# Performance work log

Hardware: AMD Instinct MI355X
Metric: run time of the kernel (lower is better)

The kernel has to match this reference:

```python
import jax, jax.numpy as jnp
import numpy as np

B, N, H, D, MAXH, MRP = 64, 197, 12, 64, 16, 14  # batch, tokens (14x14+cls), heads, head_dim, supernet max heads, max rel pos
TABLE = 2 * MRP + 2  # 30 rows per table


def setup_inputs() -> dict:
    key = jax.random.key(0)
    ks = jax.random.split(key, 5)
    x = jax.random.normal(ks[0], (B, N, 3 * D * MAXH), dtype=jnp.float32)
    mk = lambda k: (0.02 * jax.random.normal(k, (TABLE, D), dtype=jnp.float32))
    return {"x": x, "tk_v": mk(ks[1]), "tk_h": mk(ks[2]), "tv_v": mk(ks[3]), "tv_h": mk(ks[4])}


def _rel_pos_emb(table_v, table_h, n):
    # RelativePosition2D_super.forward(length_q=n, length_k=n)
    lq = n - 1
    s = int(np.sqrt(lq))  # 14
    r = jnp.arange(lq)
    dv = r[None, :] // s - r[:, None] // s
    dh = r[None, :] % s - r[:, None] % s
    iv = jnp.clip(dv, -MRP, MRP) + MRP + 1
    ih = jnp.clip(dh, -MRP, MRP) + MRP + 1
    iv = jnp.pad(iv, ((1, 0), (1, 0)))  # CLS row/col -> index 0
    ih = jnp.pad(ih, ((1, 0), (1, 0)))
    return table_v[iv] + table_h[ih]  # (n, n, D)


def reference(x, tk_v, tk_h, tv_v, tv_h):
    scale = D ** (-0.5)  # sample_scale = 64**-0.5
    xs = x[:, :, : H * D * 3]
    qkv = xs.reshape(B, N, 3, H, D).transpose(2, 0, 3, 1, 4)  # (3,B,H,N,D)
    q, k, v = qkv[0], qkv[1], qkv[2]
    attn = jnp.einsum('bhid,bhjd->bhij', q, k) * scale
    rk = _rel_pos_emb(tk_v, tk_h, N)  # (N,N,D)
    attn = attn + jnp.einsum('bhid,ijd->bhij', q, rk) * scale
    attn = jax.nn.softmax(attn, axis=-1)  # attn_drop p=0.0 -> identity
    out = jnp.einsum('bhij,bhjd->bhid', attn, v)
    rv = _rel_pos_emb(tv_v, tv_h, N)  # (N,N,D)
    out = out + jnp.einsum('bhij,ijd->bhid', attn, rv)
    out = out.transpose(0, 2, 1, 3).reshape(B, N, H * D)  # (B,N,768)
    return jnp.pad(out, ((0, 0), (0, 0), (0, MAXH * D - H * D)))  # pad to (B,N,1024)
```

## Files before the change

kernel.cpp:

```cpp
#include <hip/hip_runtime.h>

typedef float  f4v   __attribute__((ext_vector_type(4)));
typedef float  f32x4 __attribute__((ext_vector_type(4)));
typedef short  s8v   __attribute__((ext_vector_type(8)));
typedef short  s4v   __attribute__((ext_vector_type(4)));
typedef __bf16 bf16x8 __attribute__((ext_vector_type(8)));

#define N_   197
#define H_   12
#define CIN  3072
#define COUT 1024
#define VSTR 296
#define ASTR 72
#define BSTR 40

#define MEMBAR() asm volatile("" ::: "memory")

__device__ __forceinline__ unsigned short f2bf(float f) {
    unsigned u = __float_as_uint(f);
    u += 0x7FFFu + ((u >> 16) & 1u);
    return (unsigned short)(u >> 16);
}
__device__ __forceinline__ float bf2f(unsigned short s) {
    return __uint_as_float(((unsigned)s) << 16);
}
__device__ __forceinline__ f32x4 mfma_bf16(s8v a, s8v b, f32x4 c) {
    return __builtin_amdgcn_mfma_f32_16x16x32_bf16(
        __builtin_bit_cast(bf16x8, a), __builtin_bit_cast(bf16x8, b), c, 0, 0, 0);
}
__device__ __forceinline__ void st4f(volatile unsigned short* p, float a, float b, float c, float d) {
    s4v v;
    v[0] = (short)f2bf(a); v[1] = (short)f2bf(b);
    v[2] = (short)f2bf(c); v[3] = (short)f2bf(d);
    *(volatile s4v*)p = v;
}
__device__ __forceinline__ void st4z(volatile unsigned short* p) {
    s4v v = {0, 0, 0, 0};
    *(volatile s4v*)p = v;
}

__launch_bounds__(1024, 4)
__global__ void attn_super(const float* __restrict__ x,
                           const float* __restrict__ tkv,
                           const float* __restrict__ tkh,
                           const float* __restrict__ tvv,
                           const float* __restrict__ tvh,
                           float* __restrict__ out) {
    __shared__ __align__(16) unsigned short Kl[272 * 72];
    __shared__ __align__(16) unsigned short Vt[64 * VSTR];
    __shared__ __align__(16) unsigned short AR[16][16 * ASTR];
    __shared__ __align__(16) unsigned short INDv[16 * 224];
    __shared__ __align__(16) unsigned short INDh[16 * 224];
    __shared__ __align__(16) unsigned short Bext[224 * BSTR];

    const int bid = blockIdx.x;
    const int b = bid / H_, h = bid % H_;
    const int tid = threadIdx.x;
    const int w  = tid >> 6;
    const int l  = tid & 63;
    const int lg = l >> 4;
    const int ln = l & 15;

    const float* xb = x + (size_t)b * N_ * CIN;

    if (h < 4) {
        float* oz = out + (size_t)b * N_ * COUT + 768 + h * 64;
        for (int idx = tid; idx < N_ * 16; idx += 1024) {
            int row = idx >> 4, c4 = idx & 15;
            f4v z = {0.f, 0.f, 0.f, 0.f};
            *(f4v*)(oz + (size_t)row * COUT + c4 * 4) = z;
        }
    }

    f4v kr[5];
    #pragma unroll
    for (int it = 0; it < 5; ++it) {
        int idx = it * 1024 + tid;
        bool a5 = (it < 4) || (tid < 256);
        int row = idx >> 4, d0 = (idx & 15) * 4;
        f4v v = {0.f, 0.f, 0.f, 0.f};
        if (a5) {
            if (row < N_)                     v = *(const f4v*)(xb + (size_t)row * CIN + 768 + h * 64 + d0);
            else if (row >= 208 && row < 238) v = *(const f4v*)(tkv + (row - 208) * 64 + d0);
            else if (row >= 240 && row < 270) v = *(const f4v*)(tkh + (row - 240) * 64 + d0);
        }
        kr[it] = v;
    }
    f4v q1[2], q2[2];
    if (w < 13) {
        int qrow = w * 16 + ln; if (qrow > 196) qrow = 196;
        const float* qp = xb + (size_t)qrow * CIN + h * 64;
        #pragma unroll
        for (int s2 = 0; s2 < 2; ++s2) {
            q1[s2] = *(const f4v*)(qp + s2 * 32 + lg * 8);
            q2[s2] = *(const f4v*)(qp + s2 * 32 + lg * 8 + 4);
        }
    }
    f4v vr[5];
    #pragma unroll
    for (int it = 0; it < 5; ++it) {
        int idx = it * 1024 + tid;
        bool a5 = (it < 4) || (tid < 512);
        int j = idx % 288, d0 = (idx / 288) * 4;
        f4v v = {0.f, 0.f, 0.f, 0.f};
        if (a5) {
            if (j < N_)                     v = *(const f4v*)(xb + (size_t)j * CIN + 1536 + h * 64 + d0);
            else if (j >= 224 && j < 254)   v = *(const f4v*)(tvv + (j - 224) * 64 + d0);
            else if (j >= 256 && j < 286)   v = *(const f4v*)(tvh + (j - 256) * 64 + d0);
        }
        vr[it] = v;
    }

    #pragma unroll
    for (int it = 0; it < 5; ++it) {
        int idx = it * 1024 + tid;
        bool a5 = (it < 4) || (tid < 256);
        if (a5) {
            int row = idx >> 4, d0 = (idx & 15) * 4;
            f4v v = kr[it];
            s4v pk;
            pk[0] = (short)f2bf(v[0]); pk[1] = (short)f2bf(v[1]);
            pk[2] = (short)f2bf(v[2]); pk[3] = (short)f2bf(v[3]);
            *(s4v*)(&Kl[row * 72 + d0]) = pk;
        }
    }
    for (int idx = tid; idx < 16 * 224; idx += 1024) {
        int m = idx / 224, k = idx % 224;
        int km1 = k - 1;
        bool kv = (k >= 1 && k <= 196);
        INDv[idx] = (kv && (km1 / 14) == m) ? (unsigned short)0x3F80 : (unsigned short)0;
        INDh[idx] = (kv && (km1 % 14) == m) ? (unsigned short)0x3F80 : (unsigned short)0;
    }
    for (int idx = tid; idx < 224 * 32; idx += 1024) {
        int k = idx >> 5, c = idx & 31;
        unsigned short v = 0;
        if (k >= 1 && k <= 196) {
            int mj = (k - 1) / 14, cj = (k - 1) - mj * 14;
            if (c == mj || c == 16 + cj) v = (unsigned short)0x3F80;
        } else if (k == 0) {
            if (c == 15 || c == 31) v = (unsigned short)0x3F80;
        }
        Bext[k * BSTR + c] = v;
    }
    __syncthreads();

    const int tile = w, qb = tile * 16;
    const unsigned short* ar = &AR[w][0];
    volatile unsigned short* arv = &AR[w][0];

    f32x4 S[13];
    float rsq[4], p0q[4];
    int ritq[4], citq[4];
    if (w < 13) {
        const int iL  = qb + ln;
        const int im1 = (iL > 0) ? iL - 1 : 0;
        const int rit = im1 / 14;
        const int cit = im1 - rit * 14;

        s8v aq[2];
        #pragma unroll
        for (int s2 = 0; s2 < 2; ++s2) {
            #pragma unroll
            for (int e = 0; e < 4; ++e) {
                aq[s2][e]     = (short)f2bf(q1[s2][e] * 0.125f);
                aq[s2][e + 4] = (short)f2bf(q2[s2][e] * 0.125f);
            }
        }
        float spv = 0.f, sph = 0.f;
        #pragma unroll
        for (int tt = 0; tt < 4; ++tt) {
            f32x4 acc = {0.f, 0.f, 0.f, 0.f};
            #pragma unroll
            for (int s2 = 0; s2 < 2; ++s2) {
                const s8v bk = *(const s8v*)(&Kl[((13 + tt) * 16 + ln) * 72 + s2 * 32 + lg * 8]);
                acc = mfma_bf16(bk, aq[s2], acc);
            }
            const bool isV  = (tt < 2);
            const int mbase = (tt & 1) * 16;
            const int shift = isV ? rit : cit;
            const int cbase = isV ? 0 : 16;
            const bool skip0 = (tile == 0 && ln == 0);
            #pragma unroll
            for (int r = 0; r < 4; ++r) {
                int m = mbase + 4 * lg + r;
                int t = m + shift - 15;
                if (!skip0 && m < 30 && t >= 0 && t < 15)
                    arv[ln * ASTR + cbase + t] = f2bf(acc[r]);
                if (!skip0 && m == 0)
                    arv[ln * ASTR + cbase + 15] = f2bf(acc[r]);
            }
            if (tile == 0 && l == 0) {
                if (tt == 0) spv = acc[0];
                if (tt == 2) sph = acc[0];
            }
        }
        if (tile == 0 && l == 0) {
            unsigned short v0 = f2bf(spv), h0 = f2bf(sph);
            #pragma unroll
            for (int t = 0; t < 16; ++t) {
                arv[t] = v0;
                arv[16 + t] = h0;
            }
        }
        MEMBAR();
        const s8v aq2 = *(const s8v*)(&ar[ln * ASTR + lg * 8]);
        #pragma unroll
        for (int ct = 0; ct < 13; ++ct) {
            const s8v be = *(const s8v*)(&Bext[(ct * 16 + ln) * BSTR + lg * 8]);
            f32x4 acc = {0.f, 0.f, 0.f, 0.f};
            acc = mfma_bf16(be, aq2, acc);
            #pragma unroll
            for (int s2 = 0; s2 < 2; ++s2) {
                const s8v bk = *(const s8v*)(&Kl[(ct * 16 + ln) * 72 + s2 * 32 + lg * 8]);
                acc = mfma_bf16(bk, aq[s2], acc);
            }
            S[ct] = acc;
        }
    }
    #pragma unroll
    for (int it = 0; it < 5; ++it) {
        int idx = it * 1024 + tid;
        bool a5 = (it < 4) || (tid < 512);
        if (a5) {
            int j = idx % 288, d0 = (idx / 288) * 4;
            f4v v = vr[it];
            #pragma unroll
            for (int e = 0; e < 4; ++e)
                Vt[(d0 + e) * VSTR + j] = f2bf(v[e]);
        }
    }

    if (w < 13) {
        float rs4[4] = {0.f, 0.f, 0.f, 0.f};
        #pragma unroll
        for (int ct = 0; ct < 13; ++ct) {
            #pragma unroll
            for (int r = 0; r < 4; ++r) {
                float p = __expf(S[ct][r]);
                if (ct == 12) { if (4 * lg + r > 4) p = 0.f; }
                S[ct][r] = p;
                rs4[r] += p;
            }
        }
        float rs = (rs4[0] + rs4[1]) + (rs4[2] + rs4[3]);
        rs += __shfl_xor(rs, 16);
        rs += __shfl_xor(rs, 32);
        float p00 = S[0][0];
        #pragma unroll
        for (int r = 0; r < 4; ++r) {
            rsq[r] = __shfl(rs,  4 * lg + r);
            p0q[r] = __shfl(p00, 4 * lg + r);
        }
        #pragma unroll
        for (int r = 0; r < 4; ++r) {
            int qr2 = qb + 4 * lg + r;
            int im  = (qr2 > 0) ? qr2 - 1 : 0;
            ritq[r] = im / 14;
            citq[r] = im - ritq[r] * 14;
        }
    }
    __syncthreads();

    if (w >= 13) return;

    f32x4 oacc[4];
    #pragma unroll
    for (int nt = 0; nt < 4; ++nt) { f32x4 z = {0.f,0.f,0.f,0.f}; oacc[nt] = z; }
    f32x4 cwv = {0.f,0.f,0.f,0.f}, cwh = {0.f,0.f,0.f,0.f};

    #pragma unroll
    for (int win = 0; win < 3; ++win) {
        MEMBAR();
        #pragma unroll
        for (int cc = 0; cc < 4; ++cc) {
            int ct = win * 4 + cc;
            st4f(&arv[ln * ASTR + cc * 16 + 4 * lg], S[ct][0], S[ct][1], S[ct][2], S[ct][3]);
        }
        MEMBAR();
        #pragma unroll
        for (int kk = 0; kk < 2; ++kk) {
            int kt = win * 2 + kk;
            const s8v ap = *(const s8v*)(&ar[ln * ASTR + kk * 32 + lg * 8]);
            #pragma unroll
            for (int nt = 0; nt < 4; ++nt) {
                const s8v bv = *(const s8v*)(&Vt[(nt * 16 + ln) * VSTR + kt * 32 + lg * 8]);
                oacc[nt] = mfma_bf16(ap, bv, oacc[nt]);
            }
            const s8v bi = *(const s8v*)(&INDv[ln * 224 + kt * 32 + lg * 8]);
            cwv = mfma_bf16(ap, bi, cwv);
            const s8v bh = *(const s8v*)(&INDh[ln * 224 + kt * 32 + lg * 8]);
            cwh = mfma_bf16(ap, bh, cwh);
        }
    }
    {
        MEMBAR();
        st4f(&arv[ln * ASTR + 4 * lg], S[12][0], S[12][1], S[12][2], S[12][3]);
        st4z(&arv[ln * ASTR + 16 + 4 * lg]);
        st4z(&arv[ln * ASTR + 32 + lg * 8]);
        st4z(&arv[ln * ASTR + 36 + lg * 8]);
        MEMBAR();
        {
            const s8v ap = *(const s8v*)(&ar[ln * ASTR + lg * 8]);
            #pragma unroll
            for (int nt = 0; nt < 4; ++nt) {
                const s8v bv = *(const s8v*)(&Vt[(nt * 16 + ln) * VSTR + 192 + lg * 8]);
                oacc[nt] = mfma_bf16(ap, bv, oacc[nt]);
            }
            const s8v bi = *(const s8v*)(&INDv[ln * 224 + 192 + lg * 8]);
            cwv = mfma_bf16(ap, bi, cwv);
            const s8v bh = *(const s8v*)(&INDh[ln * 224 + 192 + lg * 8]);
            cwh = mfma_bf16(ap, bh, cwh);
        }
        MEMBAR();
        #pragma unroll
        for (int r = 0; r < 4; ++r) {
            int q = 4 * lg + r;
            bool isRow0 = (tile == 0) && (q == 0);
            if (ln <= 13 && !isRow0)
                arv[q * ASTR + 47 + ln - ritq[r]] = f2bf(cwv[r]);
            if (ln == 15)
                arv[q * ASTR + 32] = f2bf(isRow0 ? rsq[r] : p0q[r]);
        }
        MEMBAR();
        {
            const s8v ap = *(const s8v*)(&ar[ln * ASTR + 32 + lg * 8]);
            #pragma unroll
            for (int nt = 0; nt < 4; ++nt) {
                const s8v bv = *(const s8v*)(&Vt[(nt * 16 + ln) * VSTR + 224 + lg * 8]);
                oacc[nt] = mfma_bf16(ap, bv, oacc[nt]);
            }
        }
    }
    {
        MEMBAR();
        st4z(&arv[ln * ASTR + lg * 8]);
        st4z(&arv[ln * ASTR + 4 + lg * 8]);
        MEMBAR();
        #pragma unroll
        for (int r = 0; r < 4; ++r) {
            int q = 4 * lg + r;
            bool isRow0 = (tile == 0) && (q == 0);
            if (ln <= 13 && !isRow0)
                arv[q * ASTR + 15 + ln - citq[r]] = f2bf(cwh[r]);
            if (ln == 15)
                arv[q * ASTR + 0] = f2bf(isRow0 ? rsq[r] : p0q[r]);
        }
        MEMBAR();
        {
            const s8v ap = *(const s8v*)(&ar[ln * ASTR + lg * 8]);
            #pragma unroll
            for (int nt = 0; nt < 4; ++nt) {
                const s8v bv = *(const s8v*)(&Vt[(nt * 16 + ln) * VSTR + 256 + lg * 8]);
                oacc[nt] = mfma_bf16(ap, bv, oacc[nt]);
            }
        }
    }
    #pragma unroll
    for (int r = 0; r < 4; ++r) {
        int n = qb + 4 * lg + r;
        if (n < N_) {
            float sc = 1.0f / rsq[r];
            float* orow = out + ((size_t)b * N_ + n) * COUT + h * 64;
            #pragma unroll
            for (int nt = 0; nt < 4; ++nt)
                orow[nt * 16 + ln] = oacc[nt][r] * sc;
        }
    }
}

extern "C" void kernel_launch(void* const* d_in, const int* in_sizes, int n_in,
                              void* d_out, int out_size, void* d_ws, size_t ws_size,
                              hipStream_t stream) {
    const float* x   = (const float*)d_in[0];
    const float* tkv = (const float*)d_in[1];
    const float* tkh = (const float*)d_in[2];
    const float* tvv = (const float*)d_in[3];
    const float* tvh = (const float*)d_in[4];
    float* o = (float*)d_out;
    attn_super<<<dim3(64 * H_), dim3(1024), 0, stream>>>(x, tkv, tkh, tvv, tvh, o);
}
```

Measured before the change: 71.65 us.

## Make attention kernel persistent with prefetch of next head's Q/K/V

```diff
diff --git a/kernel.cpp b/kernel.cpp
--- a/kernel.cpp
+++ b/kernel.cpp
@@ -24,14 +24,17 @@
 __device__ __forceinline__ float bf2f(unsigned short s) {
     return __uint_as_float(((unsigned)s) << 16);
 }
+__device__ __forceinline__ unsigned pk2(float a, float b) {
+    return (unsigned)f2bf(a) | ((unsigned)f2bf(b) << 16);
+}
 __device__ __forceinline__ f32x4 mfma_bf16(s8v a, s8v b, f32x4 c) {
     return __builtin_amdgcn_mfma_f32_16x16x32_bf16(
         __builtin_bit_cast(bf16x8, a), __builtin_bit_cast(bf16x8, b), c, 0, 0, 0);
 }
-__device__ __forceinline__ void st4f(volatile unsigned short* p, float a, float b, float c, float d) {
+__device__ __forceinline__ void st4p(volatile unsigned short* p, unsigned u0, unsigned u1) {
     s4v v;
-    v[0] = (short)f2bf(a); v[1] = (short)f2bf(b);
-    v[2] = (short)f2bf(c); v[3] = (short)f2bf(d);
+    v[0] = (short)(u0 & 0xFFFF); v[1] = (short)(u0 >> 16);
+    v[2] = (short)(u1 & 0xFFFF); v[3] = (short)(u1 >> 16);
     *(volatile s4v*)p = v;
 }
 __device__ __forceinline__ void st4z(volatile unsigned short* p) {
@@ -54,76 +57,12 @@
     __shared__ __align__(16) unsigned short Bext[224 * BSTR];
 
     const int bid = blockIdx.x;
-    const int b = bid / H_, h = bid % H_;
     const int tid = threadIdx.x;
     const int w  = tid >> 6;
     const int l  = tid & 63;
     const int lg = l >> 4;
     const int ln = l & 15;
 
-    const float* xb = x + (size_t)b * N_ * CIN;
-
-    if (h < 4) {
-        float* oz = out + (size_t)b * N_ * COUT + 768 + h * 64;
-        for (int idx = tid; idx < N_ * 16; idx += 1024) {
-            int row = idx >> 4, c4 = idx & 15;
-            f4v z = {0.f, 0.f, 0.f, 0.f};
-            *(f4v*)(oz + (size_t)row * COUT + c4 * 4) = z;
-        }
-    }
-
-    f4v kr[5];
-    #pragma unroll
-    for (int it = 0; it < 5; ++it) {
-        int idx = it * 1024 + tid;
-        bool a5 = (it < 4) || (tid < 256);
-        int row = idx >> 4, d0 = (idx & 15) * 4;
-        f4v v = {0.f, 0.f, 0.f, 0.f};
-        if (a5) {
-            if (row < N_)                     v = *(const f4v*)(xb + (size_t)row * CIN + 768 + h * 64 + d0);
-            else if (row >= 208 && row < 238) v = *(const f4v*)(tkv + (row - 208) * 64 + d0);
-            else if (row >= 240 && row < 270) v = *(const f4v*)(tkh + (row - 240) * 64 + d0);
-        }
-        kr[it] = v;
-    }
-    f4v q1[2], q2[2];
-    if (w < 13) {
-        int qrow = w * 16 + ln; if (qrow > 196) qrow = 196;
-        const float* qp = xb + (size_t)qrow * CIN + h * 64;
-        #pragma unroll
-        for (int s2 = 0; s2 < 2; ++s2) {
-            q1[s2] = *(const f4v*)(qp + s2 * 32 + lg * 8);
-            q2[s2] = *(const f4v*)(qp + s2 * 32 + lg * 8 + 4);
-        }
-    }
-    f4v vr[5];
-    #pragma unroll
-    for (int it = 0; it < 5; ++it) {
-        int idx = it * 1024 + tid;
-        bool a5 = (it < 4) || (tid < 512);
-        int j = idx % 288, d0 = (idx / 288) * 4;
-        f4v v = {0.f, 0.f, 0.f, 0.f};
-        if (a5) {
-            if (j < N_)                     v = *(const f4v*)(xb + (size_t)j * CIN + 1536 + h * 64 + d0);
-            else if (j >= 224 && j < 254)   v = *(const f4v*)(tvv + (j - 224) * 64 + d0);
-            else if (j >= 256 && j < 286)   v = *(const f4v*)(tvh + (j - 256) * 64 + d0);
-        }
-        vr[it] = v;
-    }
-
-    #pragma unroll
-    for (int it = 0; it < 5; ++it) {
-        int idx = it * 1024 + tid;
-        bool a5 = (it < 4) || (tid < 256);
-        if (a5) {
-            int row = idx >> 4, d0 = (idx & 15) * 4;
-            f4v v = kr[it];
-            s4v pk;
-            pk[0] = (short)f2bf(v[0]); pk[1] = (short)f2bf(v[1]);
-            pk[2] = (short)f2bf(v[2]); pk[3] = (short)f2bf(v[3]);
-            *(s4v*)(&Kl[row * 72 + d0]) = pk;
-        }
-    }
     for (int idx = tid; idx < 16 * 224; idx += 1024) {
         int m = idx / 224, k = idx % 224;
         int km1 = k - 1;
@@ -142,229 +81,366 @@
         }
         Bext[k * BSTR + c] = v;
     }
+
+    f4v kr[5];
+    f4v q1[2], q2[2];
+    f4v vr[5];
+    {
+        int pair = bid;
+        int b = pair / H_, h = pair - b * H_;
+        const float* xb = x + (size_t)b * N_ * CIN;
+        #pragma unroll
+        for (int it = 0; it < 5; ++it) {
+            int idx = it * 1024 + tid;
+            bool a5 = (it < 4) || (tid < 256);
+            int row = idx >> 4, d0 = (idx & 15) * 4;
+            f4v v = {0.f, 0.f, 0.f, 0.f};
+            if (a5) {
+                if (row < N_)                     v = *(const f4v*)(xb + (size_t)row * CIN + 768 + h * 64 + d0);
+                else if (row >= 208 && row < 238) v = *(const f4v*)(tkv + (row - 208) * 64 + d0);
+                else if (row >= 240 && row < 270) v = *(const f4v*)(tkh + (row - 240) * 64 + d0);
+            }
+            kr[it] = v;
+        }
+        if (w < 13) {
+            int qrow = w * 16 + ln; if (qrow > 196) qrow = 196;
+            const float* qp = xb + (size_t)qrow * CIN + h * 64;
+            #pragma unroll
+            for (int s2 = 0; s2 < 2; ++s2) {
+                q1[s2] = *(const f4v*)(qp + s2 * 32 + lg * 8);
+                q2[s2] = *(const f4v*)(qp + s2 * 32 + lg * 8 + 4);
+            }
+        }
+        #pragma unroll
+        for (int it = 0; it < 5; ++it) {
+            int idx = it * 1024 + tid;
+            bool a5 = (it < 4) || (tid < 256);
+            if (a5) {
+                int row = idx >> 4, d0 = (idx & 15) * 4;
+                f4v v = kr[it];
+                s4v pk;
+                pk[0] = (short)f2bf(v[0]); pk[1] = (short)f2bf(v[1]);
+                pk[2] = (short)f2bf(v[2]); pk[3] = (short)f2bf(v[3]);
+                *(s4v*)(&Kl[row * 72 + d0]) = pk;
+            }
+        }
+        #pragma unroll
+        for (int it = 0; it < 5; ++it) {
+            int idx = it * 1024 + tid;
+            bool a5 = (it < 4) || (tid < 512);
+            int j = idx % 288, d0 = (idx / 288) * 4;
+            f4v v = {0.f, 0.f, 0.f, 0.f};
+            if (a5) {
+                if (j < N_)                     v = *(const f4v*)(xb + (size_t)j * CIN + 1536 + h * 64 + d0);
+                else if (j >= 224 && j < 254)   v = *(const f4v*)(tvv + (j - 224) * 64 + d0);
+                else if (j >= 256 && j < 286)   v = *(const f4v*)(tvh + (j - 256) * 64 + d0);
+            }
+            vr[it] = v;
+        }
+    }
     __syncthreads();
 
     const int tile = w, qb = tile * 16;
     const unsigned short* ar = &AR[w][0];
     volatile unsigned short* arv = &AR[w][0];
 
-    f32x4 S[13];
-    float rsq[4], p0q[4];
-    int ritq[4], citq[4];
-    if (w < 13) {
-        const int iL  = qb + ln;
-        const int im1 = (iL > 0) ? iL - 1 : 0;
-        const int rit = im1 / 14;
-        const int cit = im1 - rit * 14;
-
-        s8v aq[2];
+    for (int i = 0; i < 3; ++i) {
+        const int pair = i * 256 + bid;
+        const int b = pair / H_, h = pair - b * H_;
+        const float* xb = x + (size_t)b * N_ * CIN;
+
+        if (h < 4) {
+            float* oz = out + (size_t)b * N_ * COUT + 768 + h * 64;
+            for (int idx = tid; idx < N_ * 16; idx += 1024) {
+                int row = idx >> 4, c4 = idx & 15;
+                f4v z = {0.f, 0.f, 0.f, 0.f};
+                *(f4v*)(oz + (size_t)row * COUT + c4 * 4) = z;
+            }
+        }
+
+        unsigned pp[13][2];
+        float rsq[4], p0q[4];
+        int ritq[4], citq[4];
+
+        if (w < 13) {
+            const int iL  = qb + ln;
+            const int im1 = (iL > 0) ? iL - 1 : 0;
+            const int rit = im1 / 14;
+            const int cit = im1 - rit * 14;
+
+            s8v aq[2];
+            #pragma unroll
+            for (int s2 = 0; s2 < 2; ++s2) {
+                #pragma unroll
+                for (int e = 0; e < 4; ++e) {
+                    aq[s2][e]     = (short)f2bf(q1[s2][e] * 0.125f);
+                    aq[s2][e + 4] = (short)f2bf(q2[s2][e] * 0.125f);
+                }
+            }
+            float spv = 0.f, sph = 0.f;
+            #pragma unroll
+            for (int tt = 0; tt < 4; ++tt) {
+                f32x4 acc = {0.f, 0.f, 0.f, 0.f};
+                #pragma unroll
+                for (int s2 = 0; s2 < 2; ++s2) {
+                    const s8v bk = *(const s8v*)(&Kl[((13 + tt) * 16 + ln) * 72 + s2 * 32 + lg * 8]);
+                    acc = mfma_bf16(bk, aq[s2], acc);
+                }
+                const bool isV  = (tt < 2);
+                const int mbase = (tt & 1) * 16;
+                const int shift = isV ? rit : cit;
+                const int cbase = isV ? 0 : 16;
+                const bool skip0 = (tile == 0 && ln == 0);
+                #pragma unroll
+                for (int r = 0; r < 4; ++r) {
+                    int m = mbase + 4 * lg + r;
+                    int t = m + shift - 15;
+                    if (!skip0 && m < 30 && t >= 0 && t < 15)
+                        arv[ln * ASTR + cbase + t] = f2bf(acc[r]);
+                    if (!skip0 && m == 0)
+                        arv[ln * ASTR + cbase + 15] = f2bf(acc[r]);
+                }
+                if (tile == 0 && l == 0) {
+                    if (tt == 0) spv = acc[0];
+                    if (tt == 2) sph = acc[0];
+                }
+            }
+            if (tile == 0 && l == 0) {
+                unsigned short v0 = f2bf(spv), h0 = f2bf(sph);
+                #pragma unroll
+                for (int t = 0; t < 16; ++t) {
+                    arv[t] = v0;
+                    arv[16 + t] = h0;
+                }
+            }
+            MEMBAR();
+            const s8v aq2 = *(const s8v*)(&ar[ln * ASTR + lg * 8]);
+            f32x4 S[13];
+            #pragma unroll
+            for (int ct = 0; ct < 13; ++ct) {
+                const s8v be = *(const s8v*)(&Bext[(ct * 16 + ln) * BSTR + lg * 8]);
+                f32x4 acc = {0.f, 0.f, 0.f, 0.f};
+                acc = mfma_bf16(be, aq2, acc);
+                #pragma unroll
+                for (int s2 = 0; s2 < 2; ++s2) {
+                    const s8v bk = *(const s8v*)(&Kl[(ct * 16 + ln) * 72 + s2 * 32 + lg * 8]);
+                    acc = mfma_bf16(bk, aq[s2], acc);
+                }
+                S[ct] = acc;
+            }
+            float rs4[4] = {0.f, 0.f, 0.f, 0.f};
+            float p00 = 0.f;
+            #pragma unroll
+            for (int ct = 0; ct < 13; ++ct) {
+                float pv[4];
+                #pragma unroll
+                for (int r = 0; r < 4; ++r) {
+                    float p = __expf(S[ct][r]);
+                    if (ct == 12) { if (4 * lg + r > 4) p = 0.f; }
+                    pv[r] = p;
+                    rs4[r] += p;
+                }
+                if (ct == 0) p00 = pv[0];
+                pp[ct][0] = pk2(pv[0], pv[1]);
+                pp[ct][1] = pk2(pv[2], pv[3]);
+            }
+            float rs = (rs4[0] + rs4[1]) + (rs4[2] + rs4[3]);
+            rs += __shfl_xor(rs, 16);
+            rs += __shfl_xor(rs, 32);
+            #pragma unroll
+            for (int r = 0; r < 4; ++r) {
+                rsq[r] = __shfl(rs,  4 * lg + r);
+                p0q[r] = __shfl(p00, 4 * lg + r);
+            }
+            #pragma unroll
+            for (int r = 0; r < 4; ++r) {
+                int qr2 = qb + 4 * lg + r;
+                int im  = (qr2 > 0) ? qr2 - 1 : 0;
+                ritq[r] = im / 14;
+                citq[r] = im - ritq[r] * 14;
+            }
+        }
         #pragma unroll
-        for (int s2 = 0; s2 < 2; ++s2) {
-            #pragma unroll
-            for (int e = 0; e < 4; ++e) {
-                aq[s2][e]     = (short)f2bf(q1[s2][e] * 0.125f);
-                aq[s2][e + 4] = (short)f2bf(q2[s2][e] * 0.125f);
-            }
-        }
-        float spv = 0.f, sph = 0.f;
+        for (int it = 0; it < 5; ++it) {
+            int idx = it * 1024 + tid;
+            bool a5 = (it < 4) || (tid < 512);
+            if (a5) {
+                int j = idx % 288, d0 = (idx / 288) * 4;
+                f4v v = vr[it];
+                #pragma unroll
+                for (int e = 0; e < 4; ++e)
+                    Vt[(d0 + e) * VSTR + j] = f2bf(v[e]);
+            }
+        }
+        if (i < 2) {
+            const int np = (i + 1) * 256 + bid;
+            const int nb = np / H_, nh = np - nb * H_;
+            const float* nxb = x + (size_t)nb * N_ * CIN;
+            #pragma unroll
+            for (int it = 0; it < 5; ++it) {
+                int idx = it * 1024 + tid;
+                bool a5 = (it < 4) || (tid < 256);
+                int row = idx >> 4, d0 = (idx & 15) * 4;
+                f4v v = {0.f, 0.f, 0.f, 0.f};
+                if (a5) {
+                    if (row < N_)                     v = *(const f4v*)(nxb + (size_t)row * CIN + 768 + nh * 64 + d0);
+                    else if (row >= 208 && row < 238) v = *(const f4v*)(tkv + (row - 208) * 64 + d0);
+                    else if (row >= 240 && row < 270) v = *(const f4v*)(tkh + (row - 240) * 64 + d0);
+                }
+                kr[it] = v;
+            }
+            if (w < 13) {
+                int qrow = w * 16 + ln; if (qrow > 196) qrow = 196;
+                const float* qp = nxb + (size_t)qrow * CIN + nh * 64;
+                #pragma unroll
+                for (int s2 = 0; s2 < 2; ++s2) {
+                    q1[s2] = *(const f4v*)(qp + s2 * 32 + lg * 8);
+                    q2[s2] = *(const f4v*)(qp + s2 * 32 + lg * 8 + 4);
+                }
+            }
+        }
+        __syncthreads();
+
+        if (w < 13) {
+            f32x4 oacc[4];
+            #pragma unroll
+            for (int nt = 0; nt < 4; ++nt) { f32x4 z = {0.f,0.f,0.f,0.f}; oacc[nt] = z; }
+            f32x4 cwv = {0.f,0.f,0.f,0.f}, cwh = {0.f,0.f,0.f,0.f};
+
+            #pragma unroll
+            for (int win = 0; win < 3; ++win) {
+                MEMBAR();
+                #pragma unroll
+                for (int cc = 0; cc < 4; ++cc) {
+                    int ct = win * 4 + cc;
+                    st4p(&arv[ln * ASTR + cc * 16 + 4 * lg], pp[ct][0], pp[ct][1]);
+                }
+                MEMBAR();
+                #pragma unroll
+                for (int kk = 0; kk < 2; ++kk) {
+                    int kt = win * 2 + kk;
+                    const s8v ap = *(const s8v*)(&ar[ln * ASTR + kk * 32 + lg * 8]);
+                    #pragma unroll
+                    for (int nt = 0; nt < 4; ++nt) {
+                        const s8v bv = *(const s8v*)(&Vt[(nt * 16 + ln) * VSTR + kt * 32 + lg * 8]);
+                        oacc[nt] = mfma_bf16(ap, bv, oacc[nt]);
+                    }
+                    const s8v bi = *(const s8v*)(&INDv[ln * 224 + kt * 32 + lg * 8]);
+                    cwv = mfma_bf16(ap, bi, cwv);
+                    const s8v bh = *(const s8v*)(&INDh[ln * 224 + kt * 32 + lg * 8]);
+                    cwh = mfma_bf16(ap, bh, cwh);
+                }
+            }
+            {
+                MEMBAR();
+                st4p(&arv[ln * ASTR + 4 * lg], pp[12][0], pp[12][1]);
+                st4z(&arv[ln * ASTR + 16 + 4 * lg]);
+                st4z(&arv[ln * ASTR + 32 + lg * 8]);
+                st4z(&arv[ln * ASTR + 36 + lg * 8]);
+                MEMBAR();
+                {
+                    const s8v ap = *(const s8v*)(&ar[ln * ASTR + lg * 8]);
+                    #pragma unroll
+                    for (int nt = 0; nt < 4; ++nt) {
+                        const s8v bv = *(const s8v*)(&Vt[(nt * 16 + ln) * VSTR + 192 + lg * 8]);
+                        oacc[nt] = mfma_bf16(ap, bv, oacc[nt]);
+                    }
+                    const s8v bi = *(const s8v*)(&INDv[ln * 224 + 192 + lg * 8]);
+                    cwv = mfma_bf16(ap, bi, cwv);
+                    const s8v bh = *(const s8v*)(&INDh[ln * 224 + 192 + lg * 8]);
+                    cwh = mfma_bf16(ap, bh, cwh);
+                }
+                MEMBAR();
+                #pragma unroll
+                for (int r = 0; r < 4; ++r) {
+                    int q = 4 * lg + r;
+                    bool isRow0 = (tile == 0) && (q == 0);
+                    if (ln <= 13 && !isRow0)
+                        arv[q * ASTR + 47 + ln - ritq[r]] = f2bf(cwv[r]);
+                    if (ln == 15)
+                        arv[q * ASTR + 32] = f2bf(isRow0 ? rsq[r] : p0q[r]);
+                }
+                MEMBAR();
+                {
+                    const s8v ap = *(const s8v*)(&ar[ln * ASTR + 32 + lg * 8]);
+                    #pragma unroll
+                    for (int nt = 0; nt < 4; ++nt) {
+                        const s8v bv = *(const s8v*)(&Vt[(nt * 16 + ln) * VSTR + 224 + lg * 8]);
+                        oacc[nt] = mfma_bf16(ap, bv, oacc[nt]);
+                    }
+                }
+            }
+            {
+                MEMBAR();
+                st4z(&arv[ln * ASTR + lg * 8]);
+                st4z(&arv[ln * ASTR + 4 + lg * 8]);
+                MEMBAR();
+                #pragma unroll
+                for (int r = 0; r < 4; ++r) {
+                    int q = 4 * lg + r;
+                    bool isRow0 = (tile == 0) && (q == 0);
+                    if (ln <= 13 && !isRow0)
+                        arv[q * ASTR + 15 + ln - citq[r]] = f2bf(cwh[r]);
+                    if (ln == 15)
+                        arv[q * ASTR + 0] = f2bf(isRow0 ? rsq[r] : p0q[r]);
+                }
+                MEMBAR();
+                {
+                    const s8v ap = *(const s8v*)(&ar[ln * ASTR + lg * 8]);
+                    #pragma unroll
+                    for (int nt = 0; nt < 4; ++nt) {
+                        const s8v bv = *(const s8v*)(&Vt[(nt * 16 + ln) * VSTR + 256 + lg * 8]);
+                        oacc[nt] = mfma_bf16(ap, bv, oacc[nt]);
+                    }
+                }
+            }
+            #pragma unroll
+            for (int r = 0; r < 4; ++r) {
+                int n = qb + 4 * lg + r;
+                if (n < N_) {
+                    float sc = 1.0f / rsq[r];
+                    float* orow = out + ((size_t)b * N_ + n) * COUT + h * 64;
+                    #pragma unroll
+                    for (int nt = 0; nt < 4; ++nt)
+                        orow[nt * 16 + ln] = oacc[nt][r] * sc;
+                }
+            }
+        }
+
+        if (i == 2) break;
+
         #pragma unroll
-        for (int tt = 0; tt < 4; ++tt) {
-            f32x4 acc = {0.f, 0.f, 0.f, 0.f};
-            #pragma unroll
-            for (int s2 = 0; s2 < 2; ++s2) {
-                const s8v bk = *(const s8v*)(&Kl[((13 + tt) * 16 + ln) * 72 + s2 * 32 + lg * 8]);
-                acc = mfma_bf16(bk, aq[s2], acc);
-            }
-            const bool isV  = (tt < 2);
-            const int mbase = (tt & 1) * 16;
-            const int shift = isV ? rit : cit;
-            const int cbase = isV ? 0 : 16;
-            const bool skip0 = (tile == 0 && ln == 0);
-            #pragma unroll
-            for (int r = 0; r < 4; ++r) {
-                int m = mbase + 4 * lg + r;
-                int t = m + shift - 15;
-                if (!skip0 && m < 30 && t >= 0 && t < 15)
-                    arv[ln * ASTR + cbase + t] = f2bf(acc[r]);
-                if (!skip0 && m == 0)
-                    arv[ln * ASTR + cbase + 15] = f2bf(acc[r]);
-            }
-            if (tile == 0 && l == 0) {
-                if (tt == 0) spv = acc[0];
-                if (tt == 2) sph = acc[0];
-            }
-        }
-        if (tile == 0 && l == 0) {
-            unsigned short v0 = f2bf(spv), h0 = f2bf(sph);
-            #pragma unroll
-            for (int t = 0; t < 16; ++t) {
-                arv[t] = v0;
-                arv[16 + t] = h0;
-            }
-        }
-        MEMBAR();
-        const s8v aq2 = *(const s8v*)(&ar[ln * ASTR + lg * 8]);
-        #pragma unroll
-        for (int ct = 0; ct < 13; ++ct) {
-            const s8v be = *(const s8v*)(&Bext[(ct * 16 + ln) * BSTR + lg * 8]);
-            f32x4 acc = {0.f, 0.f, 0.f, 0.f};
-            acc = mfma_bf16(be, aq2, acc);
-            #pragma unroll
-            for (int s2 = 0; s2 < 2; ++s2) {
-                const s8v bk = *(const s8v*)(&Kl[(ct * 16 + ln) * 72 + s2 * 32 + lg * 8]);
-                acc = mfma_bf16(bk, aq[s2], acc);
-            }
-            S[ct] = acc;
-        }
-    }
-    #pragma unroll
-    for (int it = 0; it < 5; ++it) {
-        int idx = it * 1024 + tid;
-        bool a5 = (it < 4) || (tid < 512);
-        if (a5) {
-            int j = idx % 288, d0 = (idx / 288) * 4;
-            f4v v = vr[it];
-            #pragma unroll
-            for (int e = 0; e < 4; ++e)
-                Vt[(d0 + e) * VSTR + j] = f2bf(v[e]);
-        }
-    }
-
-    if (w < 13) {
-        float rs4[4] = {0.f, 0.f, 0.f, 0.f};
-        #pragma unroll
-        for (int ct = 0; ct < 13; ++ct) {
-            #pragma unroll
-            for (int r = 0; r < 4; ++r) {
-                float p = __expf(S[ct][r]);
-                if (ct == 12) { if (4 * lg + r > 4) p = 0.f; }
-                S[ct][r] = p;
-                rs4[r] += p;
-            }
-        }
-        float rs = (rs4[0] + rs4[1]) + (rs4[2] + rs4[3]);
-        rs += __shfl_xor(rs, 16);
-        rs += __shfl_xor(rs, 32);
-        float p00 = S[0][0];
-        #pragma unroll
-        for (int r = 0; r < 4; ++r) {
-            rsq[r] = __shfl(rs,  4 * lg + r);
-            p0q[r] = __shfl(p00, 4 * lg + r);
-        }
-        #pragma unroll
-        for (int r = 0; r < 4; ++r) {
-            int qr2 = qb + 4 * lg + r;
-            int im  = (qr2 > 0) ? qr2 - 1 : 0;
-            ritq[r] = im / 14;
-            citq[r] = im - ritq[r] * 14;
-        }
-    }
-    __syncthreads();
-
-    if (w >= 13) return;
-
-    f32x4 oacc[4];
-    #pragma unroll
-    for (int nt = 0; nt < 4; ++nt) { f32x4 z = {0.f,0.f,0.f,0.f}; oacc[nt] = z; }
-    f32x4 cwv = {0.f,0.f,0.f,0.f}, cwh = {0.f,0.f,0.f,0.f};
-
-    #pragma unroll
-    for (int win = 0; win < 3; ++win) {
-        MEMBAR();
-        #pragma unroll
-        for (int cc = 0; cc < 4; ++cc) {
-            int ct = win * 4 + cc;
-            st4f(&arv[ln * ASTR + cc * 16 + 4 * lg], S[ct][0], S[ct][1], S[ct][2], S[ct][3]);
-        }
-        MEMBAR();
-        #pragma unroll
-        for (int kk = 0; kk < 2; ++kk) {
-            int kt = win * 2 + kk;
-            const s8v ap = *(const s8v*)(&ar[ln * ASTR + kk * 32 + lg * 8]);
-            #pragma unroll
-            for (int nt = 0; nt < 4; ++nt) {
-                const s8v bv = *(const s8v*)(&Vt[(nt * 16 + ln) * VSTR + kt * 32 + lg * 8]);
-                oacc[nt] = mfma_bf16(ap, bv, oacc[nt]);
-            }
-            const s8v bi = *(const s8v*)(&INDv[ln * 224 + kt * 32 + lg * 8]);
-            cwv = mfma_bf16(ap, bi, cwv);
-            const s8v bh = *(const s8v*)(&INDh[ln * 224 + kt * 32 + lg * 8]);
-            cwh = mfma_bf16(ap, bh, cwh);
-        }
-    }
-    {
-        MEMBAR();
-        st4f(&arv[ln * ASTR + 4 * lg], S[12][0], S[12][1], S[12][2], S[12][3]);
-        st4z(&arv[ln * ASTR + 16 + 4 * lg]);
-        st4z(&arv[ln * ASTR + 32 + lg * 8]);
-        st4z(&arv[ln * ASTR + 36 + lg * 8]);
-        MEMBAR();
+        for (int it = 0; it < 5; ++it) {
+            int idx = it * 1024 + tid;
+            bool a5 = (it < 4) || (tid < 256);
+            if (a5) {
+                int row = idx >> 4, d0 = (idx & 15) * 4;
+                f4v v = kr[it];
+                s4v pk;
+                pk[0] = (short)f2bf(v[0]); pk[1] = (short)f2bf(v[1]);
+                pk[2] = (short)f2bf(v[2]); pk[3] = (short)f2bf(v[3]);
+                *(s4v*)(&Kl[row * 72 + d0]) = pk;
+            }
+        }
         {
-            const s8v ap = *(const s8v*)(&ar[ln * ASTR + lg * 8]);
-            #pragma unroll
-            for (int nt = 0; nt < 4; ++nt) {
-                const s8v bv = *(const s8v*)(&Vt[(nt * 16 + ln) * VSTR + 192 + lg * 8]);
-                oacc[nt] = mfma_bf16(ap, bv, oacc[nt]);
-            }
-            const s8v bi = *(const s8v*)(&INDv[ln * 224 + 192 + lg * 8]);
-            cwv = mfma_bf16(ap, bi, cwv);
-            const s8v bh = *(const s8v*)(&INDh[ln * 224 + 192 + lg * 8]);
-            cwh = mfma_bf16(ap, bh, cwh);
-        }
-        MEMBAR();
-        #pragma unroll
-        for (int r = 0; r < 4; ++r) {
-            int q = 4 * lg + r;
-            bool isRow0 = (tile == 0) && (q == 0);
-            if (ln <= 13 && !isRow0)
-                arv[q * ASTR + 47 + ln - ritq[r]] = f2bf(cwv[r]);
-            if (ln == 15)
-                arv[q * ASTR + 32] = f2bf(isRow0 ? rsq[r] : p0q[r]);
-        }
-        MEMBAR();
-        {
-            const s8v ap = *(const s8v*)(&ar[ln * ASTR + 32 + lg * 8]);
-            #pragma unroll
-            for (int nt = 0; nt < 4; ++nt) {
-                const s8v bv = *(const s8v*)(&Vt[(nt * 16 + ln) * VSTR + 224 + lg * 8]);
-                oacc[nt] = mfma_bf16(ap, bv, oacc[nt]);
-            }
-        }
-    }
-    {
-        MEMBAR();
-        st4z(&arv[ln * ASTR + lg * 8]);
-        st4z(&arv[ln * ASTR + 4 + lg * 8]);
-        MEMBAR();
-        #pragma unroll
-        for (int r = 0; r < 4; ++r) {
-            int q = 4 * lg + r;
-            bool isRow0 = (tile == 0) && (q == 0);
-            if (ln <= 13 && !isRow0)
-                arv[q * ASTR + 15 + ln - citq[r]] = f2bf(cwh[r]);
-            if (ln == 15)
-                arv[q * ASTR + 0] = f2bf(isRow0 ? rsq[r] : p0q[r]);
-        }
-        MEMBAR();
-        {
-            const s8v ap = *(const s8v*)(&ar[ln * ASTR + lg * 8]);
-            #pragma unroll
-            for (int nt = 0; nt < 4; ++nt) {
-                const s8v bv = *(const s8v*)(&Vt[(nt * 16 + ln) * VSTR + 256 + lg * 8]);
-                oacc[nt] = mfma_bf16(ap, bv, oacc[nt]);
-            }
-        }
-    }
-    #pragma unroll
-    for (int r = 0; r < 4; ++r) {
-        int n = qb + 4 * lg + r;
-        if (n < N_) {
-            float sc = 1.0f / rsq[r];
-            float* orow = out + ((size_t)b * N_ + n) * COUT + h * 64;
-            #pragma unroll
-            for (int nt = 0; nt < 4; ++nt)
-                orow[nt * 16 + ln] = oacc[nt][r] * sc;
-        }
+            const int np = (i + 1) * 256 + bid;
+            const int nb = np / H_, nh = np - nb * H_;
+            const float* nxb = x + (size_t)nb * N_ * CIN;
+            #pragma unroll
+            for (int it = 0; it < 5; ++it) {
+                int idx = it * 1024 + tid;
+                bool a5 = (it < 4) || (tid < 512);
+                int j = idx % 288, d0 = (idx / 288) * 4;
+                f4v v = {0.f, 0.f, 0.f, 0.f};
+                if (a5) {
+                    if (j < N_)                     v = *(const f4v*)(nxb + (size_t)j * CIN + 1536 + nh * 64 + d0);
+                    else if (j >= 224 && j < 254)   v = *(const f4v*)(tvv + (j - 224) * 64 + d0);
+                    else if (j >= 256 && j < 286)   v = *(const f4v*)(tvh + (j - 256) * 64 + d0);
+                }
+                vr[it] = v;
+            }
+        }
+        __syncthreads();
     }
 }
 
@@ -377,5 +453,5 @@
     const float* tvv = (const float*)d_in[3];
     const float* tvh = (const float*)d_in[4];
     float* o = (float*)d_out;
-    attn_super<<<dim3(64 * H_), dim3(1024), 0, stream>>>(x, tkv, tkh, tvv, tvh, o);
-}
+    attn_super<<<dim3(256), dim3(1024), 0, stream>>>(x, tkv, tkh, tvv, tvh, o);
+}
```

After: 224.8 us. 3.14x slower.

## Precompute indicator tables in global workspace and vectorize V transpose stores

Applied to the files above, without the earlier changes.

```diff
diff --git a/kernel.cpp b/kernel.cpp
--- a/kernel.cpp
+++ b/kernel.cpp
@@ -13,6 +13,8 @@
 #define VSTR 296
 #define ASTR 72
 #define BSTR 40
+#define G_INDV 8960
+#define G_INDH 12544
 
 #define MEMBAR() asm volatile("" ::: "memory")
 
@@ -37,6 +39,34 @@
 __device__ __forceinline__ void st4z(volatile unsigned short* p) {
     s4v v = {0, 0, 0, 0};
     *(volatile s4v*)p = v;
+}
+
+__global__ void init_tabs(unsigned short* __restrict__ g) {
+    int idx = blockIdx.x * 256 + threadIdx.x;
+    if (idx >= 16128) return;
+    unsigned short v = 0;
+    if (idx < 8960) {
+        int k = idx / 40, c = idx - k * 40;
+        if (c < 32) {
+            if (k >= 1 && k <= 196) {
+                int mj = (k - 1) / 14, cj = (k - 1) - mj * 14;
+                if (c == mj || c == 16 + cj) v = (unsigned short)0x3F80;
+            } else if (k == 0) {
+                if (c == 15 || c == 31) v = (unsigned short)0x3F80;
+            }
+        }
+    } else {
+        int t = idx - 8960;
+        int tab = t / 3584;
+        int r = t - tab * 3584;
+        int m = r / 224, k = r - m * 224;
+        if (k >= 1 && k <= 196) {
+            int km1 = k - 1;
+            int mk = tab ? (km1 % 14) : (km1 / 14);
+            if (mk == m) v = (unsigned short)0x3F80;
+        }
+    }
+    g[idx] = v;
 }
 
 __launch_bounds__(1024, 4)
@@ -45,13 +75,11 @@
                            const float* __restrict__ tkh,
                            const float* __restrict__ tvv,
                            const float* __restrict__ tvh,
+                           const unsigned short* __restrict__ gt,
                            float* __restrict__ out) {
     __shared__ __align__(16) unsigned short Kl[272 * 72];
     __shared__ __align__(16) unsigned short Vt[64 * VSTR];
     __shared__ __align__(16) unsigned short AR[16][16 * ASTR];
-    __shared__ __align__(16) unsigned short INDv[16 * 224];
-    __shared__ __align__(16) unsigned short INDh[16 * 224];
-    __shared__ __align__(16) unsigned short Bext[224 * BSTR];
 
     const int bid = blockIdx.x;
     const int b = bid / H_, h = bid % H_;
@@ -96,19 +124,24 @@
             q2[s2] = *(const f4v*)(qp + s2 * 32 + lg * 8 + 4);
         }
     }
-    f4v vr[5];
-    #pragma unroll
-    for (int it = 0; it < 5; ++it) {
-        int idx = it * 1024 + tid;
-        bool a5 = (it < 4) || (tid < 512);
-        int j = idx % 288, d0 = (idx / 288) * 4;
-        f4v v = {0.f, 0.f, 0.f, 0.f};
-        if (a5) {
-            if (j < N_)                     v = *(const f4v*)(xb + (size_t)j * CIN + 1536 + h * 64 + d0);
-            else if (j >= 224 && j < 254)   v = *(const f4v*)(tvv + (j - 224) * 64 + d0);
-            else if (j >= 256 && j < 286)   v = *(const f4v*)(tvh + (j - 256) * 64 + d0);
-        }
-        vr[it] = v;
+    f4v vr4[2][4];
+    #pragma unroll
+    for (int it = 0; it < 2; ++it) {
+        int item = it * 1024 + tid;
+        bool act = (it == 0) || (tid < 128);
+        int dg = item / 72, jg = item - dg * 72;
+        int d0 = dg * 4, j0 = jg * 4;
+        #pragma unroll
+        for (int jj = 0; jj < 4; ++jj) {
+            int j = j0 + jj;
+            f4v v = {0.f, 0.f, 0.f, 0.f};
+            if (act) {
+                if (j < N_)                     v = *(const f4v*)(xb + (size_t)j * CIN + 1536 + h * 64 + d0);
+                else if (j >= 224 && j < 254)   v = *(const f4v*)(tvv + (j - 224) * 64 + d0);
+                else if (j >= 256 && j < 286)   v = *(const f4v*)(tvh + (j - 256) * 64 + d0);
+            }
+            vr4[it][jj] = v;
+        }
     }
 
     #pragma unroll
@@ -124,24 +157,6 @@
             *(s4v*)(&Kl[row * 72 + d0]) = pk;
         }
     }
-    for (int idx = tid; idx < 16 * 224; idx += 1024) {
-        int m = idx / 224, k = idx % 224;
-        int km1 = k - 1;
-        bool kv = (k >= 1 && k <= 196);
-        INDv[idx] = (kv && (km1 / 14) == m) ? (unsigned short)0x3F80 : (unsigned short)0;
-        INDh[idx] = (kv && (km1 % 14) == m) ? (unsigned short)0x3F80 : (unsigned short)0;
-    }
-    for (int idx = tid; idx < 224 * 32; idx += 1024) {
-        int k = idx >> 5, c = idx & 31;
-        unsigned short v = 0;
-        if (k >= 1 && k <= 196) {
-            int mj = (k - 1) / 14, cj = (k - 1) - mj * 14;
-            if (c == mj || c == 16 + cj) v = (unsigned short)0x3F80;
-        } else if (k == 0) {
-            if (c == 15 || c == 31) v = (unsigned short)0x3F80;
-        }
-        Bext[k * BSTR + c] = v;
-    }
     __syncthreads();
 
     const int tile = w, qb = tile * 16;
@@ -206,7 +221,7 @@
         const s8v aq2 = *(const s8v*)(&ar[ln * ASTR + lg * 8]);
         #pragma unroll
         for (int ct = 0; ct < 13; ++ct) {
-            const s8v be = *(const s8v*)(&Bext[(ct * 16 + ln) * BSTR + lg * 8]);
+            const s8v be = *(const s8v*)(&gt[(ct * 16 + ln) * BSTR + lg * 8]);
             f32x4 acc = {0.f, 0.f, 0.f, 0.f};
             acc = mfma_bf16(be, aq2, acc);
             #pragma unroll
@@ -218,15 +233,21 @@
         }
     }
     #pragma unroll
-    for (int it = 0; it < 5; ++it) {
-        int idx = it * 1024 + tid;
-        bool a5 = (it < 4) || (tid < 512);
-        if (a5) {
-            int j = idx % 288, d0 = (idx / 288) * 4;
-            f4v v = vr[it];
-            #pragma unroll
-            for (int e = 0; e < 4; ++e)
-                Vt[(d0 + e) * VSTR + j] = f2bf(v[e]);
+    for (int it = 0; it < 2; ++it) {
+        int item = it * 1024 + tid;
+        bool act = (it == 0) || (tid < 128);
+        if (act) {
+            int dg = item / 72, jg = item - dg * 72;
+            int d0 = dg * 4, j0 = jg * 4;
+            #pragma unroll
+            for (int e = 0; e < 4; ++e) {
+                s4v wv_;
+                wv_[0] = (short)f2bf(vr4[it][0][e]);
+                wv_[1] = (short)f2bf(vr4[it][1][e]);
+                wv_[2] = (short)f2bf(vr4[it][2][e]);
+                wv_[3] = (short)f2bf(vr4[it][3][e]);
+                *(s4v*)(&Vt[(d0 + e) * VSTR + j0]) = wv_;
+            }
         }
     }
 
@@ -286,9 +307,9 @@
                 const s8v bv = *(const s8v*)(&Vt[(nt * 16 + ln) * VSTR + kt * 32 + lg * 8]);
                 oacc[nt] = mfma_bf16(ap, bv, oacc[nt]);
             }
-            const s8v bi = *(const s8v*)(&INDv[ln * 224 + kt * 32 + lg * 8]);
+            const s8v bi = *(const s8v*)(&gt[G_INDV + ln * 224 + kt * 32 + lg * 8]);
             cwv = mfma_bf16(ap, bi, cwv);
-            const s8v bh = *(const s8v*)(&INDh[ln * 224 + kt * 32 + lg * 8]);
+            const s8v bh = *(const s8v*)(&gt[G_INDH + ln * 224 + kt * 32 + lg * 8]);
             cwh = mfma_bf16(ap, bh, cwh);
         }
     }
@@ -306,9 +327,9 @@
                 const s8v bv = *(const s8v*)(&Vt[(nt * 16 + ln) * VSTR + 192 + lg * 8]);
                 oacc[nt] = mfma_bf16(ap, bv, oacc[nt]);
             }
-            const s8v bi = *(const s8v*)(&INDv[ln * 224 + 192 + lg * 8]);
+            const s8v bi = *(const s8v*)(&gt[G_INDV + ln * 224 + 192 + lg * 8]);
             cwv = mfma_bf16(ap, bi, cwv);
-            const s8v bh = *(const s8v*)(&INDh[ln * 224 + 192 + lg * 8]);
+            const s8v bh = *(const s8v*)(&gt[G_INDH + ln * 224 + 192 + lg * 8]);
             cwh = mfma_bf16(ap, bh, cwh);
         }
         MEMBAR();
@@ -377,5 +398,7 @@
     const float* tvv = (const float*)d_in[3];
     const float* tvh = (const float*)d_in[4];
     float* o = (float*)d_out;
-    attn_super<<<dim3(64 * H_), dim3(1024), 0, stream>>>(x, tkv, tkh, tvv, tvh, o);
-}
+    unsigned short* gt = (unsigned short*)d_ws;
+    init_tabs<<<dim3(63), dim3(256), 0, stream>>>(gt);
+    attn_super<<<dim3(64 * H_), dim3(1024), 0, stream>>>(x, tkv, tkh, tvv, tvh, gt, o);
+}
```

Result: slower. 82.14 us (+14.6%).

## Pack softmax probabilities to bf16 in registers and shuffle into MFMA operands

Applied to the files above, without the earlier changes.

```diff
diff --git a/kernel.cpp b/kernel.cpp
--- a/kernel.cpp
+++ b/kernel.cpp
@@ -1,10 +1,11 @@
 #include <hip/hip_runtime.h>
 
-typedef float  f4v   __attribute__((ext_vector_type(4)));
-typedef float  f32x4 __attribute__((ext_vector_type(4)));
-typedef short  s8v   __attribute__((ext_vector_type(8)));
-typedef short  s4v   __attribute__((ext_vector_type(4)));
-typedef __bf16 bf16x8 __attribute__((ext_vector_type(8)));
+typedef float    f4v   __attribute__((ext_vector_type(4)));
+typedef float    f32x4 __attribute__((ext_vector_type(4)));
+typedef short    s8v   __attribute__((ext_vector_type(8)));
+typedef short    s4v   __attribute__((ext_vector_type(4)));
+typedef unsigned u4v   __attribute__((ext_vector_type(4)));
+typedef __bf16   bf16x8 __attribute__((ext_vector_type(8)));
 
 #define N_   197
 #define H_   12
@@ -21,18 +22,12 @@
     u += 0x7FFFu + ((u >> 16) & 1u);
     return (unsigned short)(u >> 16);
 }
-__device__ __forceinline__ float bf2f(unsigned short s) {
-    return __uint_as_float(((unsigned)s) << 16);
+__device__ __forceinline__ unsigned pk2(float a, float b) {
+    return (unsigned)f2bf(a) | ((unsigned)f2bf(b) << 16);
 }
 __device__ __forceinline__ f32x4 mfma_bf16(s8v a, s8v b, f32x4 c) {
     return __builtin_amdgcn_mfma_f32_16x16x32_bf16(
         __builtin_bit_cast(bf16x8, a), __builtin_bit_cast(bf16x8, b), c, 0, 0, 0);
-}
-__device__ __forceinline__ void st4f(volatile unsigned short* p, float a, float b, float c, float d) {
-    s4v v;
-    v[0] = (short)f2bf(a); v[1] = (short)f2bf(b);
-    v[2] = (short)f2bf(c); v[3] = (short)f2bf(d);
-    *(volatile s4v*)p = v;
 }
 __device__ __forceinline__ void st4z(volatile unsigned short* p) {
     s4v v = {0, 0, 0, 0};
@@ -148,7 +143,7 @@
     const unsigned short* ar = &AR[w][0];
     volatile unsigned short* arv = &AR[w][0];
 
-    f32x4 S[13];
+    unsigned pp[13][2];
     float rsq[4], p0q[4];
     int ritq[4], citq[4];
     if (w < 13) {
@@ -204,6 +199,8 @@
         }
         MEMBAR();
         const s8v aq2 = *(const s8v*)(&ar[ln * ASTR + lg * 8]);
+        float rs4[4] = {0.f, 0.f, 0.f, 0.f};
+        float p00 = 0.f;
         #pragma unroll
         for (int ct = 0; ct < 13; ++ct) {
             const s8v be = *(const s8v*)(&Bext[(ct * 16 + ln) * BSTR + lg * 8]);
@@ -214,7 +211,32 @@
                 const s8v bk = *(const s8v*)(&Kl[(ct * 16 + ln) * 72 + s2 * 32 + lg * 8]);
                 acc = mfma_bf16(bk, aq[s2], acc);
             }
-            S[ct] = acc;
+            float pv[4];
+            #pragma unroll
+            for (int r = 0; r < 4; ++r) {
+                float p = __expf(acc[r]);
+                if (ct == 12) { if (4 * lg + r > 4) p = 0.f; }
+                pv[r] = p;
+                rs4[r] += p;
+            }
+            if (ct == 0) p00 = pv[0];
+            pp[ct][0] = pk2(pv[0], pv[1]);
+            pp[ct][1] = pk2(pv[2], pv[3]);
+        }
+        float rs = (rs4[0] + rs4[1]) + (rs4[2] + rs4[3]);
+        rs += __shfl_xor(rs, 16);
+        rs += __shfl_xor(rs, 32);
+        #pragma unroll
+        for (int r = 0; r < 4; ++r) {
+            rsq[r] = __shfl(rs,  4 * lg + r);
+            p0q[r] = __shfl(p00, 4 * lg + r);
+        }
+        #pragma unroll
+        for (int r = 0; r < 4; ++r) {
+            int qr2 = qb + 4 * lg + r;
+            int im  = (qr2 > 0) ? qr2 - 1 : 0;
+            ritq[r] = im / 14;
+            citq[r] = im - ritq[r] * 14;
         }
     }
     #pragma unroll
@@ -229,36 +251,6 @@
                 Vt[(d0 + e) * VSTR + j] = f2bf(v[e]);
         }
     }
-
-    if (w < 13) {
-        float rs4[4] = {0.f, 0.f, 0.f, 0.f};
-        #pragma unroll
-        for (int ct = 0; ct < 13; ++ct) {
-            #pragma unroll
-            for (int r = 0; r < 4; ++r) {
-                float p = __expf(S[ct][r]);
-                if (ct == 12) { if (4 * lg + r > 4) p = 0.f; }
-                S[ct][r] = p;
-                rs4[r] += p;
-            }
-        }
-        float rs = (rs4[0] + rs4[1]) + (rs4[2] + rs4[3]);
-        rs += __shfl_xor(rs, 16);
-        rs += __shfl_xor(rs, 32);
-        float p00 = S[0][0];
-        #pragma unroll
-        for (int r = 0; r < 4; ++r) {
-            rsq[r] = __shfl(rs,  4 * lg + r);
-            p0q[r] = __shfl(p00, 4 * lg + r);
-        }
-        #pragma unroll
-        for (int r = 0; r < 4; ++r) {
-            int qr2 = qb + 4 * lg + r;
-            int im  = (qr2 > 0) ? qr2 - 1 : 0;
-            ritq[r] = im / 14;
-            citq[r] = im - ritq[r] * 14;
-        }
-    }
     __syncthreads();
 
     if (w >= 13) return;
@@ -268,86 +260,72 @@
     for (int nt = 0; nt < 4; ++nt) { f32x4 z = {0.f,0.f,0.f,0.f}; oacc[nt] = z; }
     f32x4 cwv = {0.f,0.f,0.f,0.f}, cwh = {0.f,0.f,0.f,0.f};
 
-    #pragma unroll
-    for (int win = 0; win < 3; ++win) {
+    const int aBase = (lg & 1) * 2;
+    const int srcA  = ln + 16 * aBase;
+    const int srcB  = srcA + 16;
+    const bool hi   = (lg >= 2);
+
+    #pragma unroll
+    for (int kt = 0; kt < 7; ++kt) {
+        unsigned e0 = __shfl(pp[2 * kt][0], srcA);
+        unsigned e1 = __shfl(pp[2 * kt][1], srcA);
+        unsigned e2 = __shfl(pp[2 * kt][0], srcB);
+        unsigned e3 = __shfl(pp[2 * kt][1], srcB);
+        unsigned o0, o1, o2, o3;
+        if (kt < 6) {
+            o0 = __shfl(pp[2 * kt + 1][0], srcA);
+            o1 = __shfl(pp[2 * kt + 1][1], srcA);
+            o2 = __shfl(pp[2 * kt + 1][0], srcB);
+            o3 = __shfl(pp[2 * kt + 1][1], srcB);
+        } else {
+            o0 = 0u; o1 = 0u; o2 = 0u; o3 = 0u;
+        }
+        u4v au;
+        au[0] = hi ? o0 : e0;
+        au[1] = hi ? o1 : e1;
+        au[2] = hi ? o2 : e2;
+        au[3] = hi ? o3 : e3;
+        const s8v ap = __builtin_bit_cast(s8v, au);
+        #pragma unroll
+        for (int nt = 0; nt < 4; ++nt) {
+            const s8v bv = *(const s8v*)(&Vt[(nt * 16 + ln) * VSTR + kt * 32 + lg * 8]);
+            oacc[nt] = mfma_bf16(ap, bv, oacc[nt]);
+        }
+        const s8v bi = *(const s8v*)(&INDv[ln * 224 + kt * 32 + lg * 8]);
+        cwv = mfma_bf16(ap, bi, cwv);
+        const s8v bh = *(const s8v*)(&INDh[ln * 224 + kt * 32 + lg * 8]);
+        cwh = mfma_bf16(ap, bh, cwh);
+    }
+    {
+        #pragma unroll
+        for (int jz = 0; jz < 4; ++jz)
+            st4z(&arv[ln * ASTR + lg * 16 + jz * 4]);
         MEMBAR();
         #pragma unroll
-        for (int cc = 0; cc < 4; ++cc) {
-            int ct = win * 4 + cc;
-            st4f(&arv[ln * ASTR + cc * 16 + 4 * lg], S[ct][0], S[ct][1], S[ct][2], S[ct][3]);
-        }
-        MEMBAR();
-        #pragma unroll
-        for (int kk = 0; kk < 2; ++kk) {
-            int kt = win * 2 + kk;
-            const s8v ap = *(const s8v*)(&ar[ln * ASTR + kk * 32 + lg * 8]);
-            #pragma unroll
-            for (int nt = 0; nt < 4; ++nt) {
-                const s8v bv = *(const s8v*)(&Vt[(nt * 16 + ln) * VSTR + kt * 32 + lg * 8]);
-                oacc[nt] = mfma_bf16(ap, bv, oacc[nt]);
-            }
-            const s8v bi = *(const s8v*)(&INDv[ln * 224 + kt * 32 + lg * 8]);
-            cwv = mfma_bf16(ap, bi, cwv);
-            const s8v bh = *(const s8v*)(&INDh[ln * 224 + kt * 32 + lg * 8]);
-            cwh = mfma_bf16(ap, bh, cwh);
-        }
-    }
-    {
-        MEMBAR();
-        st4f(&arv[ln * ASTR + 4 * lg], S[12][0], S[12][1], S[12][2], S[12][3]);
-        st4z(&arv[ln * ASTR + 16 + 4 * lg]);
-        st4z(&arv[ln * ASTR + 32 + lg * 8]);
-        st4z(&arv[ln * ASTR + 36 + lg * 8]);
+        for (int r = 0; r < 4; ++r) {
+            int q = 4 * lg + r;
+            bool isRow0 = (tile == 0) && (q == 0);
+            if (ln <= 13 && !isRow0) {
+                arv[q * ASTR + 15 + ln - ritq[r]] = f2bf(cwv[r]);
+                arv[q * ASTR + 47 + ln - citq[r]] = f2bf(cwh[r]);
+            }
+            if (ln == 15) {
+                unsigned short b0 = f2bf(isRow0 ? rsq[r] : p0q[r]);
+                arv[q * ASTR + 0]  = b0;
+                arv[q * ASTR + 32] = b0;
+            }
+        }
         MEMBAR();
         {
             const s8v ap = *(const s8v*)(&ar[ln * ASTR + lg * 8]);
             #pragma unroll
             for (int nt = 0; nt < 4; ++nt) {
-                const s8v bv = *(const s8v*)(&Vt[(nt * 16 + ln) * VSTR + 192 + lg * 8]);
+                const s8v bv = *(const s8v*)(&Vt[(nt * 16 + ln) * VSTR + 224 + lg * 8]);
                 oacc[nt] = mfma_bf16(ap, bv, oacc[nt]);
             }
-            const s8v bi = *(const s8v*)(&INDv[ln * 224 + 192 + lg * 8]);
-            cwv = mfma_bf16(ap, bi, cwv);
-            const s8v bh = *(const s8v*)(&INDh[ln * 224 + 192 + lg * 8]);
-            cwh = mfma_bf16(ap, bh, cwh);
-        }
-        MEMBAR();
-        #pragma unroll
-        for (int r = 0; r < 4; ++r) {
-            int q = 4 * lg + r;
-            bool isRow0 = (tile == 0) && (q == 0);
-            if (ln <= 13 && !isRow0)
-                arv[q * ASTR + 47 + ln - ritq[r]] = f2bf(cwv[r]);
-            if (ln == 15)
-                arv[q * ASTR + 32] = f2bf(isRow0 ? rsq[r] : p0q[r]);
-        }
-        MEMBAR();
+        }
         {
             const s8v ap = *(const s8v*)(&ar[ln * ASTR + 32 + lg * 8]);
-            #pragma unroll
-            for (int nt = 0; nt < 4; ++nt) {
-                const s8v bv = *(const s8v*)(&Vt[(nt * 16 + ln) * VSTR + 224 + lg * 8]);
-                oacc[nt] = mfma_bf16(ap, bv, oacc[nt]);
-            }
-        }
-    }
-    {
-        MEMBAR();
-        st4z(&arv[ln * ASTR + lg * 8]);
-        st4z(&arv[ln * ASTR + 4 + lg * 8]);
-        MEMBAR();
-        #pragma unroll
-        for (int r = 0; r < 4; ++r) {
-            int q = 4 * lg + r;
-            bool isRow0 = (tile == 0) && (q == 0);
-            if (ln <= 13 && !isRow0)
-                arv[q * ASTR + 15 + ln - citq[r]] = f2bf(cwh[r]);
-            if (ln == 15)
-                arv[q * ASTR + 0] = f2bf(isRow0 ? rsq[r] : p0q[r]);
-        }
-        MEMBAR();
-        {
-            const s8v ap = *(const s8v*)(&ar[ln * ASTR + lg * 8]);
             #pragma unroll
             for (int nt = 0; nt < 4; ++nt) {
                 const s8v bv = *(const s8v*)(&Vt[(nt * 16 + ln) * VSTR + 256 + lg * 8]);
```

New measurement: 77.48 us. 8.1% more time.
